# Performance work log

Hardware: AMD Instinct MI355X
Metric: run time of the kernel (lower is better)

The kernel has to match this reference:

```python
import jax, jax.numpy as jnp
import numpy as np

N_NODES = 100000
IN_DIM = 128
HID = 128
OUT = 64
N_EDGES = 1600000


def _glorot(key, shape):
    fan_in = shape[1]
    bound = 1.0 / np.sqrt(fan_in)
    return jax.random.uniform(key, shape, jnp.float32, -bound, bound)


def setup_inputs() -> dict:
    key = jax.random.key(0)
    ks = jax.random.split(key, 12)
    x = jax.random.normal(ks[0], (N_NODES, IN_DIM), jnp.float32)
    edge_index = jax.random.randint(ks[1], (2, N_EDGES), 0, N_NODES, jnp.int64)
    return {
        "x": x,
        "edge_index": edge_index,
        "lin_W": _glorot(ks[2], (HID, IN_DIM)),
        "lin_b": _glorot(ks[3], (1, HID))[0],
        "c1_Wl": _glorot(ks[4], (HID, HID)),
        "c1_bl": _glorot(ks[5], (1, HID))[0],
        "c1_Wr": _glorot(ks[6], (HID, HID)),
        "c2_Wl": _glorot(ks[7], (OUT, HID)),
        "c2_bl": _glorot(ks[8], (1, OUT))[0],
        "c2_Wr": _glorot(ks[9], (OUT, HID)),
    }


def _sage_conv(x, edge_index, Wl, bl, Wr):
    # PyG SAGEConv (aggr='mean'): out_i = Wl @ mean_{j in N(i)} x_j + bl + Wr @ x_i
    n = x.shape[0]
    src, dst = edge_index[0], edge_index[1]
    msg_sum = jax.ops.segment_sum(x[src], dst, num_segments=n)          # [N, d]
    deg = jax.ops.segment_sum(jnp.ones((src.shape[0],), x.dtype), dst,
                              num_segments=n)                            # [N]
    mean = msg_sum / jnp.maximum(deg, 1.0)[:, None]                      # zero-deg -> 0
    return mean @ Wl.T + bl + x @ Wr.T


def reference(x, edge_index, lin_W, lin_b, c1_Wl, c1_bl, c1_Wr, c2_Wl, c2_bl, c2_Wr):
    h = jax.nn.relu(x @ lin_W.T + lin_b)                                 # [N, HID]
    h = jax.nn.relu(_sage_conv(h, edge_index, c1_Wl, c1_bl, c1_Wr))      # [N, HID]
    h = _sage_conv(h, edge_index, c2_Wl, c2_bl, c2_Wr)                   # [N, OUT]
    return jax.nn.log_softmax(h, axis=1)
```

## Files before the change

kernel.cpp:

```cpp
#include <hip/hip_runtime.h>


#define KDIM 128
#define CH 4096
#define BSH 8
#define BCAP 8192

using bf16x8 = __attribute__((ext_vector_type(8))) short;
using f32x4  = __attribute__((ext_vector_type(4))) float;
using f32x2  = __attribute__((ext_vector_type(2))) float;

__device__ __forceinline__ unsigned short f2bf_u(float f) {
    unsigned u = __float_as_uint(f);
    u += 0x7fffu + ((u >> 16) & 1u);
    return (unsigned short)(u >> 16);
}
__device__ __forceinline__ unsigned packbf2(float a, float b) {
    return (unsigned)f2bf_u(a) | ((unsigned)f2bf_u(b) << 16);
}
__device__ __forceinline__ float bf2f(short s) {
    return __uint_as_float(((unsigned)(unsigned short)s) << 16);
}
__device__ __forceinline__ unsigned char f2fp8(float v) {
    return (unsigned char)(__builtin_amdgcn_cvt_pk_fp8_f32(v, v, 0, false) & 0xff);
}
__device__ __forceinline__ void fp8x4_acc2(unsigned uu, f32x2* a) {
    a[0] += __builtin_amdgcn_cvt_pk_f32_fp8(uu, false);
    a[1] += __builtin_amdgcn_cvt_pk_f32_fp8(uu, true);
}
__device__ __forceinline__ uint4 fp8x8_to_bf16x8(uint2 u) {
    f32x2 a0 = __builtin_amdgcn_cvt_pk_f32_fp8(u.x, false);
    f32x2 a1 = __builtin_amdgcn_cvt_pk_f32_fp8(u.x, true);
    f32x2 a2 = __builtin_amdgcn_cvt_pk_f32_fp8(u.y, false);
    f32x2 a3 = __builtin_amdgcn_cvt_pk_f32_fp8(u.y, true);
    uint4 o;
    o.x = packbf2(a0.x, a0.y); o.y = packbf2(a1.x, a1.y);
    o.z = packbf2(a2.x, a2.y); o.w = packbf2(a3.x, a3.y);
    return o;
}
__device__ __forceinline__ uint2 bf16x8_to_fp8x8(const short* p) {
    unsigned w0 = __builtin_amdgcn_cvt_pk_fp8_f32(bf2f(p[0]), bf2f(p[1]), 0, false);
    w0 = (unsigned)__builtin_amdgcn_cvt_pk_fp8_f32(bf2f(p[2]), bf2f(p[3]), (int)w0, true);
    unsigned w1 = __builtin_amdgcn_cvt_pk_fp8_f32(bf2f(p[4]), bf2f(p[5]), 0, false);
    w1 = (unsigned)__builtin_amdgcn_cvt_pk_fp8_f32(bf2f(p[6]), bf2f(p[7]), (int)w1, true);
    return uint2{w0, w1};
}

__global__ __launch_bounds__(256) void fused_front(
    const int* __restrict__ ei, int* __restrict__ hist, int E, int nwg, int NB,
    const float* __restrict__ Wc1l, const float* __restrict__ Wc1r,
    const float* __restrict__ Wc2l, const float* __restrict__ Wc2r,
    short* __restrict__ wp,
    const float* __restrict__ X, const float* __restrict__ Wlin,
    const float* __restrict__ bias, unsigned char* __restrict__ h1q, int N)
{
    __shared__ __attribute__((aligned(16))) short xa[64 * 136];
    const int bid = blockIdx.x;
    const int t = threadIdx.x;

    if (bid < nwg) {
        int* lh = (int*)xa;
        for (int b = t; b < NB; b += 256) lh[b] = 0;
        __syncthreads();
        const int e0 = bid * CH, e1 = min(E, e0 + CH);
        for (int e = e0 + t; e < e1; e += 256)
            atomicAdd(&lh[ei[E + e] >> BSH], 1);
        __syncthreads();
        for (int b = t; b < NB; b += 256) hist[b * nwg + bid] = lh[b];
        return;
    }
    if (bid < nwg + 192) {
        int idx = (bid - nwg) * 256 + t;
        const float* W; short* dst; int off, ncf;
        if (idx < 16384)      { W = Wc1l; dst = wp;         off = idx;         ncf = 8; }
        else if (idx < 32768) { W = Wc1r; dst = wp + 16384; off = idx - 16384; ncf = 8; }
        else if (idx < 40960) { W = Wc2l; dst = wp + 32768; off = idx - 32768; ncf = 4; }
        else                  { W = Wc2r; dst = wp + 40960; off = idx - 40960; ncf = 4; }
        int j    = off & 7;
        int lane = (off >> 3) & 63;
        int cf   = (off >> 9) & (ncf - 1);
        int ks   = off >> ((ncf == 8) ? 12 : 11);
        int m = cf * 16 + (lane & 15);
        int k = ks * 32 + ((lane >> 4) << 3) + j;
        dst[off] = (short)f2bf_u(W[m * KDIM + k]);
        return;
    }

    const int w = t >> 6, lane = t & 63;
    const int row0 = (bid - nwg - 192) * 64;
    const int cf0 = w * 2;

    bf16x8 bwA[4][2];
    #pragma unroll
    for (int ks = 0; ks < 4; ++ks)
        #pragma unroll
        for (int c = 0; c < 2; ++c) {
            const int m = (cf0 + c) * 16 + (lane & 15);
            const int kb = ks * 32 + ((lane >> 4) << 3);
            const float4 wa = *(const float4*)(Wlin + m * KDIM + kb);
            const float4 wb = *(const float4*)(Wlin + m * KDIM + kb + 4);
            bf16x8 r;
            r[0] = (short)f2bf_u(wa.x); r[1] = (short)f2bf_u(wa.y);
            r[2] = (short)f2bf_u(wa.z); r[3] = (short)f2bf_u(wa.w);
            r[4] = (short)f2bf_u(wb.x); r[5] = (short)f2bf_u(wb.y);
            r[6] = (short)f2bf_u(wb.z); r[7] = (short)f2bf_u(wb.w);
            bwA[ks][c] = r;
        }

    #pragma unroll
    for (int j = 0; j < 4; ++j) {
        const int sl = t + 256 * j;
        const int r = sl >> 4, s = sl & 15;
        const int gg = s ^ (r & 7);
        const int grow = min(row0 + r, N - 1);
        const float4 f0 = *(const float4*)(X + (long)grow * KDIM + gg * 8);
        const float4 f1 = *(const float4*)(X + (long)grow * KDIM + gg * 8 + 4);
        uint4 o;
        o.x = packbf2(f0.x, f0.y); o.y = packbf2(f0.z, f0.w);
        o.z = packbf2(f1.x, f1.y); o.w = packbf2(f1.z, f1.w);
        *(uint4*)(xa + r * KDIM + s * 8) = o;
    }

    f32x4 acc[4][2];
    #pragma unroll
    for (int c = 0; c < 2; ++c) {
        const float bv = bias[(cf0 + c) * 16 + (lane & 15)];
        #pragma unroll
        for (int rf = 0; rf < 4; ++rf)
            acc[rf][c] = f32x4{bv, bv, bv, bv};
    }

    __syncthreads();

    #pragma unroll
    for (int ks = 0; ks < 4; ++ks) {
        #pragma unroll
        for (int rf = 0; rf < 4; ++rf) {
            const int rl = rf * 16 + (lane & 15);
            const int s = (ks * 4 + (lane >> 4)) ^ (rl & 7);
            const bf16x8 a = *(const bf16x8*)(xa + rl * KDIM + s * 8);
            #pragma unroll
            for (int c = 0; c < 2; ++c)
                acc[rf][c] = __builtin_amdgcn_mfma_f32_16x16x32_bf16(
                    a, bwA[ks][c], acc[rf][c], 0, 0, 0);
        }
    }

    __syncthreads();
    #pragma unroll
    for (int rf = 0; rf < 4; ++rf)
        #pragma unroll
        for (int c = 0; c < 2; ++c)
            #pragma unroll
            for (int q = 0; q < 4; ++q) {
                const int r = rf * 16 + (lane >> 4) * 4 + q;
                const int col = (cf0 + c) * 16 + (lane & 15);
                xa[r * 136 + col] = (short)f2bf_u(fmaxf(acc[rf][c][q], 0.f));
            }
    __syncthreads();
    #pragma unroll
    for (int j = 0; j < 4; ++j) {
        const int sl = t + 256 * j;
        const int r = sl >> 4, ch = sl & 15;
        const int row = row0 + r;
        if (row < N)
            *(uint2*)(h1q + (long)row * KDIM + ch * 8) =
                bf16x8_to_fp8x8(xa + r * 136 + ch * 8);
    }
}


__global__ __launch_bounds__(256) void greduce(
    const int* __restrict__ in, int* __restrict__ bsum, int n)
{
    const int t = threadIdx.x;
    const int idx = blockIdx.x * 1024 + t * 4;
    int s = 0;
    if (idx + 4 <= n) {
        int4 a = *(const int4*)(in + idx);
        s = a.x + a.y + a.z + a.w;
    } else {
        #pragma unroll
        for (int k = 0; k < 4; ++k) if (idx + k < n) s += in[idx + k];
    }
    #pragma unroll
    for (int d = 1; d < 64; d <<= 1) s += __shfl_xor(s, d);
    __shared__ int ws[4];
    if ((t & 63) == 0) ws[t >> 6] = s;
    __syncthreads();
    if (t == 0) bsum[blockIdx.x] = ws[0] + ws[1] + ws[2] + ws[3];
}

__global__ __launch_bounds__(256) void scan_bsums(int* __restrict__ bsum, int nb)
{
    const int t = threadIdx.x;
    const int lane = t & 63, wid = t >> 6;
    int v = (t < nb) ? bsum[t] : 0;
    int incl = v;
    #pragma unroll
    for (int d = 1; d < 64; d <<= 1) {
        int u = __shfl_up(incl, d);
        if (lane >= d) incl += u;
    }
    __shared__ int ws[4];
    if (lane == 63) ws[wid] = incl;
    __syncthreads();
    int woff = 0;
    #pragma unroll
    for (int w = 0; w < 4; ++w) if (w < wid) woff += ws[w];
    const int excl = woff + incl - v;
    if (t <= nb) bsum[t] = excl;
}

__global__ __launch_bounds__(256) void gapply(
    int* __restrict__ io, const int* __restrict__ bsum, int n)
{
    const int t = threadIdx.x;
    const int lane = t & 63, wid = t >> 6;
    const int idx = blockIdx.x * 1024 + t * 4;
    int v[4] = {0, 0, 0, 0};
    if (idx + 4 <= n) {
        int4 a = *(const int4*)(io + idx);
        v[0] = a.x; v[1] = a.y; v[2] = a.z; v[3] = a.w;
    } else {
        #pragma unroll
        for (int k = 0; k < 4; ++k) if (idx + k < n) v[k] = io[idx + k];
    }
    const int sum = v[0] + v[1] + v[2] + v[3];
    int incl = sum;
    #pragma unroll
    for (int d = 1; d < 64; d <<= 1) {
        int u = __shfl_up(incl, d);
        if (lane >= d) incl += u;
    }
    __shared__ int ws[4];
    if (lane == 63) ws[wid] = incl;
    __syncthreads();
    int woff = 0;
    #pragma unroll
    for (int w = 0; w < 4; ++w) if (w < wid) woff += ws[w];
    int excl = bsum[blockIdx.x] + woff + (incl - sum);
    if (idx + 4 <= n) {
        int4 o;
        o.x = excl; o.y = excl + v[0]; o.z = excl + v[0] + v[1];
        o.w = excl + v[0] + v[1] + v[2];
        *(int4*)(io + idx) = o;
    } else {
        #pragma unroll
        for (int k = 0; k < 4; ++k) {
            if (idx + k < n) { io[idx + k] = excl; excl += v[k]; }
        }
    }
}

__global__ __launch_bounds__(256) void bin_scatter(
    const int* __restrict__ ei, const int* __restrict__ hist_s,
    unsigned* __restrict__ packed, int E, int nwg, int NB)
{
    __shared__ int lc[512];
    const int w = blockIdx.x, t = threadIdx.x;
    for (int b = t; b < NB; b += 256) lc[b] = hist_s[b * nwg + w];
    __syncthreads();
    const int e0 = w * CH, e1 = min(E, e0 + CH);
    for (int e = e0 + t; e < e1; e += 256) {
        const int src = ei[e];
        const int dst = ei[E + e];
        const int b = dst >> BSH;
        const int pos = atomicAdd(&lc[b], 1);
        packed[pos] = ((unsigned)(dst & 255) << 17) | (unsigned)src;
    }
}

__global__ __launch_bounds__(256) void bucket_sort(
    const unsigned* __restrict__ packed, const int* __restrict__ hist_s,
    int* __restrict__ offs, float* __restrict__ degf, int* __restrict__ perm,
    int E, int nwg, int NB, int N)
{
    __shared__ unsigned le[BCAP];
    __shared__ int lp[BCAP];
    __shared__ int lh[256], lx[256], lc[256];
    __shared__ int ws[4];
    const int b = blockIdx.x, t = threadIdx.x;
    const int bb = hist_s[b * nwg];
    const int be = (b + 1 < NB) ? hist_s[(b + 1) * nwg] : E;
    int cnt = be - bb;
    if (cnt > BCAP) cnt = BCAP;
    for (int i = t; i < cnt; i += 256) le[i] = packed[bb + i];
    lh[t] = 0;
    __syncthreads();
    for (int i = t; i < cnt; i += 256) atomicAdd(&lh[le[i] >> 17], 1);
    __syncthreads();
    const int lane = t & 63, wid = t >> 6;
    const int v = lh[t];
    int incl = v;
    #pragma unroll
    for (int d = 1; d < 64; d <<= 1) {
        int u = __shfl_up(incl, d);
        if (lane >= d) incl += u;
    }
    if (lane == 63) ws[wid] = incl;
    __syncthreads();
    int woff = 0;
    #pragma unroll
    for (int w = 0; w < 4; ++w) if (w < wid) woff += ws[w];
    const int excl = woff + incl - v;
    lx[t] = excl;
    lc[t] = excl;
    __syncthreads();
    for (int i = t; i < cnt; i += 256) {
        const unsigned p = le[i];
        const int pos = atomicAdd(&lc[p >> 17], 1);
        lp[pos] = (int)(p & 0x1FFFFu);
    }
    __syncthreads();
    for (int i = t; i < cnt; i += 256) perm[bb + i] = lp[i];
    const int node = (b << BSH) + t;
    if (node < N) {
        offs[node] = bb + lx[t];
        degf[node] = (float)v;
    }
    if (b == NB - 1 && t == 0) offs[N] = E;
}

__global__ __launch_bounds__(256) void gather_out(
    const unsigned char* __restrict__ g2q, const short* __restrict__ r2,
    const int* __restrict__ offs, const int* __restrict__ perm,
    const float* __restrict__ degf, float* __restrict__ out, int N)
{
    const int node = blockIdx.x * 32 + (threadIdx.x >> 3);
    if (node >= N) return;
    const int c = threadIdx.x & 7;
    const int b = offs[node], e = offs[node + 1];
    f32x2 acc2[4];
    #pragma unroll
    for (int q = 0; q < 4; ++q) acc2[q] = f32x2{0.f, 0.f};
    int i = b;
    for (; i + 4 <= e; i += 4) {
        const int s0 = perm[i],     s1 = perm[i + 1];
        const int s2 = perm[i + 2], s3 = perm[i + 3];
        const uint2 u0 = *(const uint2*)(g2q + (long)s0 * 64 + c * 8);
        const uint2 u1 = *(const uint2*)(g2q + (long)s1 * 64 + c * 8);
        const uint2 u2 = *(const uint2*)(g2q + (long)s2 * 64 + c * 8);
        const uint2 u3 = *(const uint2*)(g2q + (long)s3 * 64 + c * 8);
        fp8x4_acc2(u0.x, acc2 + 0);  fp8x4_acc2(u0.y, acc2 + 2);
        fp8x4_acc2(u1.x, acc2 + 0);  fp8x4_acc2(u1.y, acc2 + 2);
        fp8x4_acc2(u2.x, acc2 + 0);  fp8x4_acc2(u2.y, acc2 + 2);
        fp8x4_acc2(u3.x, acc2 + 0);  fp8x4_acc2(u3.y, acc2 + 2);
    }
    for (; i < e; ++i) {
        const uint2 u = *(const uint2*)(g2q + (long)perm[i] * 64 + c * 8);
        fp8x4_acc2(u.x, acc2 + 0);  fp8x4_acc2(u.y, acc2 + 2);
    }
    const float inv = 1.f / fmaxf(degf[node], 1.f);
    const bf16x8 rv = *(const bf16x8*)(r2 + (long)node * 64 + c * 8);
    float v[8];
    v[0] = acc2[0].x * inv + bf2f(rv[0]);
    v[1] = acc2[0].y * inv + bf2f(rv[1]);
    v[2] = acc2[1].x * inv + bf2f(rv[2]);
    v[3] = acc2[1].y * inv + bf2f(rv[3]);
    v[4] = acc2[2].x * inv + bf2f(rv[4]);
    v[5] = acc2[2].y * inv + bf2f(rv[5]);
    v[6] = acc2[3].x * inv + bf2f(rv[6]);
    v[7] = acc2[3].y * inv + bf2f(rv[7]);
    float m = v[0];
    #pragma unroll
    for (int q = 1; q < 8; ++q) m = fmaxf(m, v[q]);
    m = fmaxf(m, __shfl_xor(m, 1));
    m = fmaxf(m, __shfl_xor(m, 2));
    m = fmaxf(m, __shfl_xor(m, 4));
    float s = 0.f;
    #pragma unroll
    for (int q = 0; q < 8; ++q) s += __expf(v[q] - m);
    s += __shfl_xor(s, 1);
    s += __shfl_xor(s, 2);
    s += __shfl_xor(s, 4);
    const float L = m + __logf(s);
    float4 oa = make_float4(v[0] - L, v[1] - L, v[2] - L, v[3] - L);
    float4 ob = make_float4(v[4] - L, v[5] - L, v[6] - L, v[7] - L);
    *(float4*)(out + (long)node * 64 + c * 8) = oa;
    *(float4*)(out + (long)node * 64 + c * 8 + 4) = ob;
}

__global__ __launch_bounds__(256) void gemm_c1c2(
    const unsigned char* __restrict__ h1q, const int* __restrict__ offs,
    const int* __restrict__ perm, const float* __restrict__ degf,
    const short* __restrict__ wpA, const short* __restrict__ wpB,
    const short* __restrict__ wpL2, const short* __restrict__ wpR2,
    const float* __restrict__ bias1, const float* __restrict__ bias2,
    unsigned char* __restrict__ g2q, short* __restrict__ r2, int N)
{
    __shared__ __attribute__((aligned(16))) short xa[64 * KDIM];
    __shared__ __attribute__((aligned(16))) short xb[64 * 136];

    const int t = threadIdx.x;
    const int w = t >> 6, lane = t & 63;
    const int row0 = blockIdx.x * 64;

    {
        const int r = t >> 2;
        const int qc = t & 3;
        const int node = min(row0 + r, N - 1);
        const int b = offs[node], e = offs[node + 1];
        f32x2 a0[16];
        #pragma unroll
        for (int q = 0; q < 16; ++q) a0[q] = f32x2{0.f, 0.f};
        const unsigned char* hp = h1q + qc * 32;
        int i = b;
        for (; i + 2 <= e; i += 2) {
            const int s0 = perm[i], s1 = perm[i + 1];
            const uint4 u0 = *(const uint4*)(hp + (long)s0 * KDIM);
            const uint4 v0 = *(const uint4*)(hp + (long)s0 * KDIM + 16);
            const uint4 u1 = *(const uint4*)(hp + (long)s1 * KDIM);
            const uint4 v1 = *(const uint4*)(hp + (long)s1 * KDIM + 16);
            fp8x4_acc2(u0.x, a0 + 0);  fp8x4_acc2(u0.y, a0 + 2);
            fp8x4_acc2(u0.z, a0 + 4);  fp8x4_acc2(u0.w, a0 + 6);
            fp8x4_acc2(v0.x, a0 + 8);  fp8x4_acc2(v0.y, a0 + 10);
            fp8x4_acc2(v0.z, a0 + 12); fp8x4_acc2(v0.w, a0 + 14);
            fp8x4_acc2(u1.x, a0 + 0);  fp8x4_acc2(u1.y, a0 + 2);
            fp8x4_acc2(u1.z, a0 + 4);  fp8x4_acc2(u1.w, a0 + 6);
            fp8x4_acc2(v1.x, a0 + 8);  fp8x4_acc2(v1.y, a0 + 10);
            fp8x4_acc2(v1.z, a0 + 12); fp8x4_acc2(v1.w, a0 + 14);
        }
        if (i < e) {
            const int s0 = perm[i];
            const uint4 u0 = *(const uint4*)(hp + (long)s0 * KDIM);
            const uint4 v0 = *(const uint4*)(hp + (long)s0 * KDIM + 16);
            fp8x4_acc2(u0.x, a0 + 0);  fp8x4_acc2(u0.y, a0 + 2);
            fp8x4_acc2(u0.z, a0 + 4);  fp8x4_acc2(u0.w, a0 + 6);
            fp8x4_acc2(v0.x, a0 + 8);  fp8x4_acc2(v0.y, a0 + 10);
            fp8x4_acc2(v0.z, a0 + 12); fp8x4_acc2(v0.w, a0 + 14);
        }
        const float inv = 1.f / fmaxf(degf[node], 1.f);
        #pragma unroll
        for (int j = 0; j < 4; ++j) {
            const int slot = (qc * 4 + j) ^ (r & 7);
            uint4 o;
            o.x = packbf2(a0[4 * j + 0].x * inv, a0[4 * j + 0].y * inv);
            o.y = packbf2(a0[4 * j + 1].x * inv, a0[4 * j + 1].y * inv);
            o.z = packbf2(a0[4 * j + 2].x * inv, a0[4 * j + 2].y * inv);
            o.w = packbf2(a0[4 * j + 3].x * inv, a0[4 * j + 3].y * inv);
            *(uint4*)(xa + r * KDIM + slot * 8) = o;
        }
    }

    #pragma unroll
    for (int j = 0; j < 4; ++j) {
        const int sl = t + 256 * j;
        const int r = sl >> 4, s = sl & 15;
        const int gg = s ^ (r & 7);
        const int grow = min(row0 + r, N - 1);
        const uint2 u = *(const uint2*)(h1q + (long)grow * KDIM + gg * 8);
        *(uint4*)(xb + r * KDIM + s * 8) = fp8x8_to_bf16x8(u);
    }

    const int cf0 = w * 2;
    bf16x8 bwA[4][2], bwB[4][2];
    #pragma unroll
    for (int ks = 0; ks < 4; ++ks)
        #pragma unroll
        for (int c = 0; c < 2; ++c) {
            bwA[ks][c] = *(const bf16x8*)(wpA + (((ks * 8) + cf0 + c) * 64 + lane) * 8);
            bwB[ks][c] = *(const bf16x8*)(wpB + (((ks * 8) + cf0 + c) * 64 + lane) * 8);
        }

    f32x4 acc[4][2];
    #pragma unroll
    for (int c = 0; c < 2; ++c) {
        const float bv = bias1[(cf0 + c) * 16 + (lane & 15)];
        #pragma unroll
        for (int rf = 0; rf < 4; ++rf)
            acc[rf][c] = f32x4{bv, bv, bv, bv};
    }

    __syncthreads();

    #pragma unroll
    for (int ks = 0; ks < 4; ++ks) {
        #pragma unroll
        for (int rf = 0; rf < 4; ++rf) {
            const int rl = rf * 16 + (lane & 15);
            const int s = (ks * 4 + (lane >> 4)) ^ (rl & 7);
            const bf16x8 a = *(const bf16x8*)(xa + rl * KDIM + s * 8);
            #pragma unroll
            for (int c = 0; c < 2; ++c)
                acc[rf][c] = __builtin_amdgcn_mfma_f32_16x16x32_bf16(
                    a, bwA[ks][c], acc[rf][c], 0, 0, 0);
            const bf16x8 bb = *(const bf16x8*)(xb + rl * KDIM + s * 8);
            #pragma unroll
            for (int c = 0; c < 2; ++c)
                acc[rf][c] = __builtin_amdgcn_mfma_f32_16x16x32_bf16(
                    bb, bwB[ks][c], acc[rf][c], 0, 0, 0);
        }
    }

    __syncthreads();
    #pragma unroll
    for (int rf = 0; rf < 4; ++rf)
        #pragma unroll
        for (int c = 0; c < 2; ++c)
            #pragma unroll
            for (int q = 0; q < 4; ++q) {
                const int r = rf * 16 + (lane >> 4) * 4 + q;
                const int col = (cf0 + c) * 16 + (lane & 15);
                const int s = col >> 3;
                xa[r * KDIM + ((s ^ (r & 7)) << 3) + (col & 7)] =
                    (short)f2bf_u(fmaxf(acc[rf][c][q], 0.f));
            }

    const int side = w >> 1;
    const int cf2 = (w & 1) * 2;
    const short* wp2 = side ? wpR2 : wpL2;

    bf16x8 bw2[4][2];
    #pragma unroll
    for (int ks = 0; ks < 4; ++ks)
        #pragma unroll
        for (int c = 0; c < 2; ++c)
            bw2[ks][c] = *(const bf16x8*)(wp2 + (((ks * 4) + cf2 + c) * 64 + lane) * 8);

    f32x4 acc2[4][2];
    #pragma unroll
    for (int c = 0; c < 2; ++c) {
        const float bv = side ? bias2[(cf2 + c) * 16 + (lane & 15)] : 0.f;
        #pragma unroll
        for (int rf = 0; rf < 4; ++rf)
            acc2[rf][c] = f32x4{bv, bv, bv, bv};
    }

    __syncthreads();

    #pragma unroll
    for (int ks = 0; ks < 4; ++ks) {
        #pragma unroll
        for (int rf = 0; rf < 4; ++rf) {
            const int rl = rf * 16 + (lane & 15);
            const int s = (ks * 4 + (lane >> 4)) ^ (rl & 7);
            const bf16x8 a = *(const bf16x8*)(xa + rl * KDIM + s * 8);
            #pragma unroll
            for (int c = 0; c < 2; ++c)
                acc2[rf][c] = __builtin_amdgcn_mfma_f32_16x16x32_bf16(
                    a, bw2[ks][c], acc2[rf][c], 0, 0, 0);
        }
    }

    {
        short* et = xb + (side ? 64 * 68 : 0);
        #pragma unroll
        for (int rf = 0; rf < 4; ++rf)
            #pragma unroll
            for (int c = 0; c < 2; ++c)
                #pragma unroll
                for (int q = 0; q < 4; ++q) {
                    const int r = rf * 16 + (lane >> 4) * 4 + q;
                    const int col = (cf2 + c) * 16 + (lane & 15);
                    et[r * 68 + col] = (short)f2bf_u(acc2[rf][c][q]);
                }
    }
    __syncthreads();
    #pragma unroll
    for (int j = 0; j < 2; ++j) {
        const int sl = t + 256 * j;
        const int r = sl >> 3, ch = sl & 7;
        const int row = row0 + r;
        if (row < N)
            *(uint2*)(g2q + (long)row * 64 + ch * 8) =
                bf16x8_to_fp8x8(xb + r * 68 + ch * 8);
    }
    #pragma unroll
    for (int j = 0; j < 2; ++j) {
        const int sl = t + 256 * j;
        const int r = sl >> 3, ch = sl & 7;
        const int row = row0 + r;
        if (row < N)
            *(uint4*)(r2 + (long)row * 64 + ch * 8) =
                *(const uint4*)(xb + 64 * 68 + r * 68 + ch * 8);
    }
}

extern "C" void kernel_launch(void* const* d_in, const int* in_sizes, int n_in,
                              void* d_out, int out_size, void* d_ws, size_t ws_size,
                              hipStream_t stream) {
    const float* x     = (const float*)d_in[0];
    const int*   ei    = (const int*)d_in[1];
    const float* lin_W = (const float*)d_in[2];
    const float* lin_b = (const float*)d_in[3];
    const float* c1_Wl = (const float*)d_in[4];
    const float* c1_bl = (const float*)d_in[5];
    const float* c1_Wr = (const float*)d_in[6];
    const float* c2_Wl = (const float*)d_in[7];
    const float* c2_bl = (const float*)d_in[8];
    const float* c2_Wr = (const float*)d_in[9];
    float* out = (float*)d_out;

    const int N = in_sizes[0] / KDIM;
    const int E = in_sizes[1] / 2;

    short* r2   = (short*)d_ws;
    unsigned char* h1q = (unsigned char*)(r2 + (size_t)N * 64);
    unsigned char* g2q = h1q + (size_t)N * KDIM;
    short* wp   = (short*)(g2q + (size_t)N * 64);
    float* degf = (float*)(wp + 49152);
    int* offs   = (int*)(degf + N);
    const int nwg = (E + CH - 1) / CH;
    const int NB  = (N + 255) >> BSH;
    int* hist   = offs + (N + 1);
    int* bsum   = hist + NB * nwg;
    unsigned* packed = (unsigned*)(bsum + 256);
    int* perm   = (int*)(packed + E);

    const int nb = (N + 63) / 64;
    const int nh = NB * nwg;
    const int nsb = (nh + 1023) / 1024;

    fused_front<<<nwg + 192 + nb, 256, 0, stream>>>(
        ei, hist, E, nwg, NB,
        c1_Wl, c1_Wr, c2_Wl, c2_Wr, wp,
        x, lin_W, lin_b, h1q, N);

    greduce<<<nsb, 256, 0, stream>>>(hist, bsum, nh);
    scan_bsums<<<1, 256, 0, stream>>>(bsum, nsb);
    gapply<<<nsb, 256, 0, stream>>>(hist, bsum, nh);
    bin_scatter<<<nwg, 256, 0, stream>>>(ei, hist, packed, E, nwg, NB);
    bucket_sort<<<NB, 256, 0, stream>>>(packed, hist, offs, degf, perm, E, nwg, NB, N);

    gemm_c1c2<<<nb, 256, 0, stream>>>(
        h1q, offs, perm, degf,
        wp, wp + 16384, wp + 32768, wp + 40960,
        c1_bl, c2_bl, g2q, r2, N);

    gather_out<<<(N + 31) / 32, 256, 0, stream>>>(g2q, r2, offs, perm, degf, out, N);
}
```

Baseline: 139.5 us.

## Double gemm_c1c2 block to 512 threads and replace XOR swizzle with padded LDS

The fused conv1/conv2 GEMM kernel now launches 512 threads per 64-row block. Each thread gathers 16 bytes of a neighbor row instead of 32 and unrolls the edge loop by four, and each wave owns a single 16-column output tile. Both kernels also drop the XOR-swizzled LDS layout in favour of a row stride of 136 elements to avoid bank conflicts. The aim is more memory parallelism and latency hiding in the irregular neighbor gather, at the cost of more threads per block and possibly lower occupancy per CU.

```diff
diff --git a/kernel.cpp b/kernel.cpp
--- a/kernel.cpp
+++ b/kernel.cpp
@@ -2,6 +2,7 @@
 
 
 #define KDIM 128
+#define TSTR 136
 #define CH 4096
 #define BSH 8
 #define BCAP 8192
@@ -111,14 +112,13 @@
     for (int j = 0; j < 4; ++j) {
         const int sl = t + 256 * j;
         const int r = sl >> 4, s = sl & 15;
-        const int gg = s ^ (r & 7);
         const int grow = min(row0 + r, N - 1);
-        const float4 f0 = *(const float4*)(X + (long)grow * KDIM + gg * 8);
-        const float4 f1 = *(const float4*)(X + (long)grow * KDIM + gg * 8 + 4);
+        const float4 f0 = *(const float4*)(X + (long)grow * KDIM + s * 8);
+        const float4 f1 = *(const float4*)(X + (long)grow * KDIM + s * 8 + 4);
         uint4 o;
         o.x = packbf2(f0.x, f0.y); o.y = packbf2(f0.z, f0.w);
         o.z = packbf2(f1.x, f1.y); o.w = packbf2(f1.z, f1.w);
-        *(uint4*)(xa + r * KDIM + s * 8) = o;
+        *(uint4*)(xa + r * TSTR + s * 8) = o;
     }
 
     f32x4 acc[4][2];
@@ -137,8 +137,8 @@
         #pragma unroll
         for (int rf = 0; rf < 4; ++rf) {
             const int rl = rf * 16 + (lane & 15);
-            const int s = (ks * 4 + (lane >> 4)) ^ (rl & 7);
-            const bf16x8 a = *(const bf16x8*)(xa + rl * KDIM + s * 8);
+            const int s = ks * 4 + (lane >> 4);
+            const bf16x8 a = *(const bf16x8*)(xa + rl * TSTR + s * 8);
             #pragma unroll
             for (int c = 0; c < 2; ++c)
                 acc[rf][c] = __builtin_amdgcn_mfma_f32_16x16x32_bf16(
@@ -381,7 +381,7 @@
     *(float4*)(out + (long)node * 64 + c * 8 + 4) = ob;
 }
 
-__global__ __launch_bounds__(256) void gemm_c1c2(
+__global__ __launch_bounds__(512) void gemm_c1c2(
     const unsigned char* __restrict__ h1q, const int* __restrict__ offs,
     const int* __restrict__ perm, const float* __restrict__ degf,
     const short* __restrict__ wpA, const short* __restrict__ wpB,
@@ -389,87 +389,78 @@
     const float* __restrict__ bias1, const float* __restrict__ bias2,
     unsigned char* __restrict__ g2q, short* __restrict__ r2, int N)
 {
-    __shared__ __attribute__((aligned(16))) short xa[64 * KDIM];
-    __shared__ __attribute__((aligned(16))) short xb[64 * 136];
+    __shared__ __attribute__((aligned(16))) short xa[64 * TSTR];
+    __shared__ __attribute__((aligned(16))) short xb[64 * TSTR];
 
     const int t = threadIdx.x;
     const int w = t >> 6, lane = t & 63;
     const int row0 = blockIdx.x * 64;
 
     {
-        const int r = t >> 2;
-        const int qc = t & 3;
+        const int r = t >> 3;
+        const int qc = t & 7;
         const int node = min(row0 + r, N - 1);
         const int b = offs[node], e = offs[node + 1];
-        f32x2 a0[16];
-        #pragma unroll
-        for (int q = 0; q < 16; ++q) a0[q] = f32x2{0.f, 0.f};
-        const unsigned char* hp = h1q + qc * 32;
+        f32x2 a0[8];
+        #pragma unroll
+        for (int q = 0; q < 8; ++q) a0[q] = f32x2{0.f, 0.f};
+        const unsigned char* hp = h1q + qc * 16;
         int i = b;
-        for (; i + 2 <= e; i += 2) {
-            const int s0 = perm[i], s1 = perm[i + 1];
+        for (; i + 4 <= e; i += 4) {
+            const int s0 = perm[i],     s1 = perm[i + 1];
+            const int s2 = perm[i + 2], s3 = perm[i + 3];
             const uint4 u0 = *(const uint4*)(hp + (long)s0 * KDIM);
-            const uint4 v0 = *(const uint4*)(hp + (long)s0 * KDIM + 16);
             const uint4 u1 = *(const uint4*)(hp + (long)s1 * KDIM);
-            const uint4 v1 = *(const uint4*)(hp + (long)s1 * KDIM + 16);
+            const uint4 u2 = *(const uint4*)(hp + (long)s2 * KDIM);
+            const uint4 u3 = *(const uint4*)(hp + (long)s3 * KDIM);
             fp8x4_acc2(u0.x, a0 + 0);  fp8x4_acc2(u0.y, a0 + 2);
             fp8x4_acc2(u0.z, a0 + 4);  fp8x4_acc2(u0.w, a0 + 6);
-            fp8x4_acc2(v0.x, a0 + 8);  fp8x4_acc2(v0.y, a0 + 10);
-            fp8x4_acc2(v0.z, a0 + 12); fp8x4_acc2(v0.w, a0 + 14);
             fp8x4_acc2(u1.x, a0 + 0);  fp8x4_acc2(u1.y, a0 + 2);
             fp8x4_acc2(u1.z, a0 + 4);  fp8x4_acc2(u1.w, a0 + 6);
-            fp8x4_acc2(v1.x, a0 + 8);  fp8x4_acc2(v1.y, a0 + 10);
-            fp8x4_acc2(v1.z, a0 + 12); fp8x4_acc2(v1.w, a0 + 14);
-        }
-        if (i < e) {
-            const int s0 = perm[i];
-            const uint4 u0 = *(const uint4*)(hp + (long)s0 * KDIM);
-            const uint4 v0 = *(const uint4*)(hp + (long)s0 * KDIM + 16);
+            fp8x4_acc2(u2.x, a0 + 0);  fp8x4_acc2(u2.y, a0 + 2);
+            fp8x4_acc2(u2.z, a0 + 4);  fp8x4_acc2(u2.w, a0 + 6);
+            fp8x4_acc2(u3.x, a0 + 0);  fp8x4_acc2(u3.y, a0 + 2);
+            fp8x4_acc2(u3.z, a0 + 4);  fp8x4_acc2(u3.w, a0 + 6);
+        }
+        for (; i < e; ++i) {
+            const uint4 u0 = *(const uint4*)(hp + (long)perm[i] * KDIM);
             fp8x4_acc2(u0.x, a0 + 0);  fp8x4_acc2(u0.y, a0 + 2);
             fp8x4_acc2(u0.z, a0 + 4);  fp8x4_acc2(u0.w, a0 + 6);
-            fp8x4_acc2(v0.x, a0 + 8);  fp8x4_acc2(v0.y, a0 + 10);
-            fp8x4_acc2(v0.z, a0 + 12); fp8x4_acc2(v0.w, a0 + 14);
         }
         const float inv = 1.f / fmaxf(degf[node], 1.f);
         #pragma unroll
-        for (int j = 0; j < 4; ++j) {
-            const int slot = (qc * 4 + j) ^ (r & 7);
+        for (int j = 0; j < 2; ++j) {
             uint4 o;
             o.x = packbf2(a0[4 * j + 0].x * inv, a0[4 * j + 0].y * inv);
             o.y = packbf2(a0[4 * j + 1].x * inv, a0[4 * j + 1].y * inv);
             o.z = packbf2(a0[4 * j + 2].x * inv, a0[4 * j + 2].y * inv);
             o.w = packbf2(a0[4 * j + 3].x * inv, a0[4 * j + 3].y * inv);
-            *(uint4*)(xa + r * KDIM + slot * 8) = o;
-        }
-    }
-
-    #pragma unroll
-    for (int j = 0; j < 4; ++j) {
-        const int sl = t + 256 * j;
+            *(uint4*)(xa + r * TSTR + (qc * 2 + j) * 8) = o;
+        }
+    }
+
+    #pragma unroll
+    for (int j = 0; j < 2; ++j) {
+        const int sl = t + 512 * j;
         const int r = sl >> 4, s = sl & 15;
-        const int gg = s ^ (r & 7);
         const int grow = min(row0 + r, N - 1);
-        const uint2 u = *(const uint2*)(h1q + (long)grow * KDIM + gg * 8);
-        *(uint4*)(xb + r * KDIM + s * 8) = fp8x8_to_bf16x8(u);
-    }
-
-    const int cf0 = w * 2;
-    bf16x8 bwA[4][2], bwB[4][2];
-    #pragma unroll
-    for (int ks = 0; ks < 4; ++ks)
-        #pragma unroll
-        for (int c = 0; c < 2; ++c) {
-            bwA[ks][c] = *(const bf16x8*)(wpA + (((ks * 8) + cf0 + c) * 64 + lane) * 8);
-            bwB[ks][c] = *(const bf16x8*)(wpB + (((ks * 8) + cf0 + c) * 64 + lane) * 8);
-        }
-
-    f32x4 acc[4][2];
-    #pragma unroll
-    for (int c = 0; c < 2; ++c) {
-        const float bv = bias1[(cf0 + c) * 16 + (lane & 15)];
+        const uint2 u = *(const uint2*)(h1q + (long)grow * KDIM + s * 8);
+        *(uint4*)(xb + r * TSTR + s * 8) = fp8x8_to_bf16x8(u);
+    }
+
+    bf16x8 bwA[4], bwB[4];
+    #pragma unroll
+    for (int ks = 0; ks < 4; ++ks) {
+        bwA[ks] = *(const bf16x8*)(wpA + (((ks * 8) + w) * 64 + lane) * 8);
+        bwB[ks] = *(const bf16x8*)(wpB + (((ks * 8) + w) * 64 + lane) * 8);
+    }
+
+    f32x4 acc[4];
+    {
+        const float bv = bias1[w * 16 + (lane & 15)];
         #pragma unroll
         for (int rf = 0; rf < 4; ++rf)
-            acc[rf][c] = f32x4{bv, bv, bv, bv};
+            acc[rf] = f32x4{bv, bv, bv, bv};
     }
 
     __syncthreads();
@@ -479,17 +470,13 @@
         #pragma unroll
         for (int rf = 0; rf < 4; ++rf) {
             const int rl = rf * 16 + (lane & 15);
-            const int s = (ks * 4 + (lane >> 4)) ^ (rl & 7);
-            const bf16x8 a = *(const bf16x8*)(xa + rl * KDIM + s * 8);
-            #pragma unroll
-            for (int c = 0; c < 2; ++c)
-                acc[rf][c] = __builtin_amdgcn_mfma_f32_16x16x32_bf16(
-                    a, bwA[ks][c], acc[rf][c], 0, 0, 0);
-            const bf16x8 bb = *(const bf16x8*)(xb + rl * KDIM + s * 8);
-            #pragma unroll
-            for (int c = 0; c < 2; ++c)
-                acc[rf][c] = __builtin_amdgcn_mfma_f32_16x16x32_bf16(
-                    bb, bwB[ks][c], acc[rf][c], 0, 0, 0);
+            const int s = ks * 4 + (lane >> 4);
+            const bf16x8 a = *(const bf16x8*)(xa + rl * TSTR + s * 8);
+            acc[rf] = __builtin_amdgcn_mfma_f32_16x16x32_bf16(
+                a, bwA[ks], acc[rf], 0, 0, 0);
+            const bf16x8 bb = *(const bf16x8*)(xb + rl * TSTR + s * 8);
+            acc[rf] = __builtin_amdgcn_mfma_f32_16x16x32_bf16(
+                bb, bwB[ks], acc[rf], 0, 0, 0);
         }
     }
 
@@ -497,83 +484,64 @@
     #pragma unroll
     for (int rf = 0; rf < 4; ++rf)
         #pragma unroll
-        for (int c = 0; c < 2; ++c)
+        for (int q = 0; q < 4; ++q) {
+            const int r = rf * 16 + (lane >> 4) * 4 + q;
+            const int col = w * 16 + (lane & 15);
+            xa[r * TSTR + col] = (short)f2bf_u(fmaxf(acc[rf][q], 0.f));
+        }
+
+    const int side = w >> 2;
+    const int cf2 = w & 3;
+    const short* wp2 = side ? wpR2 : wpL2;
+
+    bf16x8 bw2[4];
+    #pragma unroll
+    for (int ks = 0; ks < 4; ++ks)
+        bw2[ks] = *(const bf16x8*)(wp2 + (((ks * 4) + cf2) * 64 + lane) * 8);
+
+    f32x4 acc2[4];
+    {
+        const float bv = side ? bias2[cf2 * 16 + (lane & 15)] : 0.f;
+        #pragma unroll
+        for (int rf = 0; rf < 4; ++rf)
+            acc2[rf] = f32x4{bv, bv, bv, bv};
+    }
+
+    __syncthreads();
+
+    #pragma unroll
+    for (int ks = 0; ks < 4; ++ks) {
+        #pragma unroll
+        for (int rf = 0; rf < 4; ++rf) {
+            const int rl = rf * 16 + (lane & 15);
+            const int s = ks * 4 + (lane >> 4);
+            const bf16x8 a = *(const bf16x8*)(xa + rl * TSTR + s * 8);
+            acc2[rf] = __builtin_amdgcn_mfma_f32_16x16x32_bf16(
+                a, bw2[ks], acc2[rf], 0, 0, 0);
+        }
+    }
+
+    {
+        short* et = xb + (side ? 64 * 68 : 0);
+        #pragma unroll
+        for (int rf = 0; rf < 4; ++rf)
             #pragma unroll
             for (int q = 0; q < 4; ++q) {
                 const int r = rf * 16 + (lane >> 4) * 4 + q;
-                const int col = (cf0 + c) * 16 + (lane & 15);
-                const int s = col >> 3;
-                xa[r * KDIM + ((s ^ (r & 7)) << 3) + (col & 7)] =
-                    (short)f2bf_u(fmaxf(acc[rf][c][q], 0.f));
+                const int col = cf2 * 16 + (lane & 15);
+                et[r * 68 + col] = (short)f2bf_u(acc2[rf][q]);
             }
-
-    const int side = w >> 1;
-    const int cf2 = (w & 1) * 2;
-    const short* wp2 = side ? wpR2 : wpL2;
-
-    bf16x8 bw2[4][2];
-    #pragma unroll
-    for (int ks = 0; ks < 4; ++ks)
-        #pragma unroll
-        for (int c = 0; c < 2; ++c)
-            bw2[ks][c] = *(const bf16x8*)(wp2 + (((ks * 4) + cf2 + c) * 64 + lane) * 8);
-
-    f32x4 acc2[4][2];
-    #pragma unroll
-    for (int c = 0; c < 2; ++c) {
-        const float bv = side ? bias2[(cf2 + c) * 16 + (lane & 15)] : 0.f;
-        #pragma unroll
-        for (int rf = 0; rf < 4; ++rf)
-            acc2[rf][c] = f32x4{bv, bv, bv, bv};
-    }
-
-    __syncthreads();
-
-    #pragma unroll
-    for (int ks = 0; ks < 4; ++ks) {
-        #pragma unroll
-        for (int rf = 0; rf < 4; ++rf) {
-            const int rl = rf * 16 + (lane & 15);
-            const int s = (ks * 4 + (lane >> 4)) ^ (rl & 7);
-            const bf16x8 a = *(const bf16x8*)(xa + rl * KDIM + s * 8);
-            #pragma unroll
-            for (int c = 0; c < 2; ++c)
-                acc2[rf][c] = __builtin_amdgcn_mfma_f32_16x16x32_bf16(
-                    a, bw2[ks][c], acc2[rf][c], 0, 0, 0);
-        }
-    }
-
+    }
+    __syncthreads();
     {
-        short* et = xb + (side ? 64 * 68 : 0);
-        #pragma unroll
-        for (int rf = 0; rf < 4; ++rf)
-            #pragma unroll
-            for (int c = 0; c < 2; ++c)
-                #pragma unroll
-                for (int q = 0; q < 4; ++q) {
-                    const int r = rf * 16 + (lane >> 4) * 4 + q;
-                    const int col = (cf2 + c) * 16 + (lane & 15);
-                    et[r * 68 + col] = (short)f2bf_u(acc2[rf][c][q]);
-                }
-    }
-    __syncthreads();
-    #pragma unroll
-    for (int j = 0; j < 2; ++j) {
-        const int sl = t + 256 * j;
-        const int r = sl >> 3, ch = sl & 7;
+        const int r = t >> 3, ch = t & 7;
         const int row = row0 + r;
-        if (row < N)
+        if (row < N) {
             *(uint2*)(g2q + (long)row * 64 + ch * 8) =
                 bf16x8_to_fp8x8(xb + r * 68 + ch * 8);
-    }
-    #pragma unroll
-    for (int j = 0; j < 2; ++j) {
-        const int sl = t + 256 * j;
-        const int r = sl >> 3, ch = sl & 7;
-        const int row = row0 + r;
-        if (row < N)
             *(uint4*)(r2 + (long)row * 64 + ch * 8) =
                 *(const uint4*)(xb + 64 * 68 + r * 68 + ch * 8);
+        }
     }
 }
 
@@ -623,7 +591,7 @@
     bin_scatter<<<nwg, 256, 0, stream>>>(ei, hist, packed, E, nwg, NB);
     bucket_sort<<<NB, 256, 0, stream>>>(packed, hist, offs, degf, perm, E, nwg, NB, N);
 
-    gemm_c1c2<<<nb, 256, 0, stream>>>(
+    gemm_c1c2<<<nb, 512, 0, stream>>>(
         h1q, offs, perm, degf,
         wp, wp + 16384, wp + 32768, wp + 40960,
         c1_bl, c2_bl, g2q, r2, N);
```

After: 135.7 us (median of 2 runs). -2.7%, faster.
